# Kernel tuning notes

Hardware: AMD Instinct MI355X
Metric: run time of the kernel (lower is better)

The kernel has to match this reference:

```python
import jax, jax.numpy as jnp
import numpy as np

EMB = 768
NH = 12
DH = EMB // NH
NORM = float(np.sqrt(DH))  # 8.0


def setup_inputs() -> dict:
    key = jax.random.key(0)
    ks = jax.random.split(key, 9)
    B, S = 1, 4096
    s = 0.02  # realistic init scale for weights
    return {
        "x": jax.random.normal(ks[0], (B, S, EMB), jnp.float32),
        "mask": jnp.ones((B, S), jnp.float32),
        "Wq": jax.random.normal(ks[1], (EMB, EMB), jnp.float32) * s,
        "bq": jnp.zeros((EMB,), jnp.float32),
        "Wk": jax.random.normal(ks[2], (EMB, EMB), jnp.float32) * s,
        "bk": jnp.zeros((EMB,), jnp.float32),
        "Wv": jax.random.normal(ks[3], (EMB, EMB), jnp.float32) * s,
        "bv": jnp.zeros((EMB,), jnp.float32),
        "Wo": jax.random.normal(ks[4], (EMB, EMB), jnp.float32) * s,
        "bo": jnp.zeros((EMB,), jnp.float32),
    }


def reference(x, mask, Wq, bq, Wk, bk, Wv, bv, Wo, bo):
    B, S, _ = x.shape
    # QKV projections (torch Linear: x @ W.T + b)
    q = x @ Wq.T + bq
    k = x @ Wk.T + bk
    v = x @ Wv.T + bv
    # split heads: b s (nh dh) -> b nh s dh
    split = lambda t: t.reshape(B, S, NH, DH).transpose(0, 2, 1, 3)
    qh, kh, vh = split(q), split(k), split(v)
    # attention scores [b, nh, s, s]
    scores = jnp.einsum("bhqd,bhkd->bhqk", qh, kh) / NORM
    # additive mask: scores -= 10000 * (1 - mask), mask broadcast over query dim
    scores = scores - 10000.0 * (1.0 - mask[:, None, None, :])
    attn = jax.nn.softmax(scores, axis=-1)
    out = jnp.einsum("bhqk,bhkd->bhqd", attn, vh)
    # b nh s dh -> b s (nh dh)
    out = out.transpose(0, 2, 1, 3).reshape(B, S, EMB)
    return out @ Wo.T + bo
```

## Files before the change

### kernel.cpp

```cpp
#include <hip/hip_runtime.h>
#include <stdint.h>
#include <stddef.h>

#define EMB 768
#define SEQ 4096
#define NH 12
#define DH 64
#define LOG2E 1.44269504f
#define NSP 2
#define SPLEN (SEQ / NSP)
#define NBLK (NH * 32 * NSP)

typedef __attribute__((ext_vector_type(8))) short short8;
typedef __attribute__((ext_vector_type(4))) short short4v;
typedef __attribute__((ext_vector_type(4))) float f32x4;
typedef __attribute__((ext_vector_type(16))) float f32x16;
typedef __attribute__((ext_vector_type(2))) unsigned int uint32x2;

static __device__ __forceinline__ unsigned short f2bf(float f) {
  union { float f; uint32_t u; } v; v.f = f;
  uint32_t u = v.u;
  return (unsigned short)((u + 0x7FFFu + ((u >> 16) & 1u)) >> 16);
}
static __device__ __forceinline__ float bf2f(unsigned short s) {
  union { uint32_t u; float f; } v; v.u = ((uint32_t)s) << 16;
  return v.f;
}

static __device__ __forceinline__ void gl_lds16(const void* g, void* l) {
  __builtin_amdgcn_global_load_lds(
      (const __attribute__((address_space(1))) uint32_t*)g,
      (__attribute__((address_space(3))) uint32_t*)l, 16, 0, 0);
}
static __device__ __forceinline__ void gl_lds4(const void* g, void* l) {
  __builtin_amdgcn_global_load_lds(
      (const __attribute__((address_space(1))) uint32_t*)g,
      (__attribute__((address_space(3))) uint32_t*)l, 4, 0, 0);
}

__global__ void prep_kernel(const float* __restrict__ x, const float* __restrict__ mask,
                            const float* __restrict__ Wq, const float* __restrict__ Wk,
                            const float* __restrict__ Wv, const float* __restrict__ Wo,
                            unsigned short* __restrict__ xb, unsigned short* __restrict__ wqb,
                            unsigned short* __restrict__ wkb, unsigned short* __restrict__ wvb,
                            unsigned short* __restrict__ wob, float* __restrict__ mb2) {
  const int y = blockIdx.y;
  if (y == 5) {
    int i = blockIdx.x * 256 + threadIdx.x;
    if (i < SEQ) mb2[i] = -80000.f * (1.f - mask[i]);
    return;
  }
  const float* in = y == 0 ? x : y == 1 ? Wq : y == 2 ? Wk : y == 3 ? Wv : Wo;
  unsigned short* out = y == 0 ? xb : y == 1 ? wqb : y == 2 ? wkb : y == 3 ? wvb : wob;
  const int n = (y == 0) ? SEQ * EMB : EMB * EMB;
  int stride = gridDim.x * blockDim.x * 4;
  for (int i = (blockIdx.x * blockDim.x + threadIdx.x) * 4; i < n; i += stride) {
    float4 v = *reinterpret_cast<const float4*>(in + i);
    ushort4 o;
    o.x = f2bf(v.x); o.y = f2bf(v.y); o.z = f2bf(v.z); o.w = f2bf(v.w);
    *reinterpret_cast<ushort4*>(out + i) = o;
  }
}

template <int OUT_F32>
static __device__ __forceinline__ void gemm64(
    const unsigned short* __restrict__ A, const unsigned short* __restrict__ W,
    const float* __restrict__ bias, void* __restrict__ Cout,
    int M, int N, int K, int bm, int bn) {
  __shared__ unsigned short Alds[64 * 64];
  __shared__ unsigned short Blds[128 * 64];
  const int t = threadIdx.x;
  const int lane = t & 63;
  const int wave = t >> 6;
  const int wr = wave >> 1, wc = wave & 1;
  const int lm = lane & 15, lg = lane >> 4;

  f32x4 acc[2][4];
#pragma unroll
  for (int i = 0; i < 2; ++i)
#pragma unroll
    for (int j = 0; j < 4; ++j) acc[i][j] = (f32x4){0.f, 0.f, 0.f, 0.f};

  const int srow = t >> 3;
  const int scsw = (t & 7) * 16;

  const int nK = K >> 6;
  for (int kt = 0; kt < nK; ++kt) {
    const int k0 = kt << 6;
#pragma unroll
    for (int i = 0; i < 2; ++i) {
      int row = i * 32 + srow;
      int cb = scsw ^ ((row & 7) << 4);
      gl_lds16(A + (size_t)(bm * 64 + row) * K + k0 + (cb >> 1),
               (char*)Alds + i * 4096 + t * 16);
    }
#pragma unroll
    for (int i = 0; i < 4; ++i) {
      int row = i * 32 + srow;
      int cb = scsw ^ ((row & 7) << 4);
      gl_lds16(W + (size_t)(bn * 128 + row) * K + k0 + (cb >> 1),
               (char*)Blds + i * 4096 + t * 16);
    }
    __syncthreads();
#pragma unroll
    for (int kk = 0; kk < 2; ++kk) {
      short8 af[2], bfr[4];
#pragma unroll
      for (int i = 0; i < 2; ++i) {
        int rowa = wr * 32 + i * 16 + lm;
        int cba = (kk * 64 + lg * 16) ^ ((rowa & 7) << 4);
        af[i] = *reinterpret_cast<const short8*>((const char*)Alds + rowa * 128 + cba);
      }
#pragma unroll
      for (int j = 0; j < 4; ++j) {
        int rowb = wc * 64 + j * 16 + lm;
        int cbb = (kk * 64 + lg * 16) ^ ((rowb & 7) << 4);
        bfr[j] = *reinterpret_cast<const short8*>((const char*)Blds + rowb * 128 + cbb);
      }
#pragma unroll
      for (int i = 0; i < 2; ++i)
#pragma unroll
        for (int j = 0; j < 4; ++j)
          acc[i][j] = __builtin_amdgcn_mfma_f32_16x16x32_bf16(af[i], bfr[j], acc[i][j], 0, 0, 0);
    }
    __syncthreads();
  }
#pragma unroll
  for (int i = 0; i < 2; ++i) {
    int row0 = bm * 64 + wr * 32 + i * 16 + lg * 4;
#pragma unroll
    for (int j = 0; j < 4; ++j) {
      int col = bn * 128 + wc * 64 + j * 16 + lm;
      float b = bias[col];
#pragma unroll
      for (int r = 0; r < 4; ++r) {
        float v = acc[i][j][r] + b;
        if (OUT_F32)
          ((float*)Cout)[(size_t)(row0 + r) * N + col] = v;
        else
          ((unsigned short*)Cout)[(size_t)(row0 + r) * N + col] = f2bf(v);
      }
    }
  }
}

__global__ __launch_bounds__(256, 2) void gemm_wo(
    const unsigned short* __restrict__ A, const unsigned short* __restrict__ W,
    const float* __restrict__ bias, float* __restrict__ C) {
  gemm64<1>(A, W, bias, C, SEQ, EMB, EMB, blockIdx.x, blockIdx.y);
}

__global__ __launch_bounds__(256, 2) void qkv_gemm(
    const unsigned short* __restrict__ A,
    const unsigned short* __restrict__ W0, const unsigned short* __restrict__ W1,
    const unsigned short* __restrict__ W2,
    const float* __restrict__ b0, const float* __restrict__ b1, const float* __restrict__ b2,
    unsigned short* __restrict__ Qo, unsigned short* __restrict__ Ko,
    unsigned short* __restrict__ Vto) {
  __shared__ unsigned short smem[12288];
  unsigned short* Alds = smem;
  unsigned short* Blds = smem + 4096;

  const int z = blockIdx.z;
  const unsigned short* W = z == 0 ? W0 : z == 1 ? W1 : W2;
  const float* bias = z == 0 ? b0 : z == 1 ? b1 : b2;
  const int bm = blockIdx.x, bn = blockIdx.y;

  const int t = threadIdx.x;
  const int lane = t & 63;
  const int wave = t >> 6;
  const int wr = wave >> 1, wc = wave & 1;
  const int lm = lane & 15, lg = lane >> 4;

  f32x4 acc[2][4];
#pragma unroll
  for (int i = 0; i < 2; ++i)
#pragma unroll
    for (int j = 0; j < 4; ++j) acc[i][j] = (f32x4){0.f, 0.f, 0.f, 0.f};

  const int srow = t >> 3;
  const int scsw = (t & 7) * 16;

  for (int kt = 0; kt < EMB / 64; ++kt) {
    const int k0 = kt << 6;
#pragma unroll
    for (int i = 0; i < 2; ++i) {
      int row = i * 32 + srow;
      int cb = scsw ^ ((row & 7) << 4);
      gl_lds16(A + (size_t)(bm * 64 + row) * EMB + k0 + (cb >> 1),
               (char*)Alds + i * 4096 + t * 16);
    }
#pragma unroll
    for (int i = 0; i < 4; ++i) {
      int row = i * 32 + srow;
      int cb = scsw ^ ((row & 7) << 4);
      gl_lds16(W + (size_t)(bn * 128 + row) * EMB + k0 + (cb >> 1),
               (char*)Blds + i * 4096 + t * 16);
    }
    __syncthreads();
#pragma unroll
    for (int kk = 0; kk < 2; ++kk) {
      short8 af[2], bfr[4];
#pragma unroll
      for (int i = 0; i < 2; ++i) {
        int rowa = wr * 32 + i * 16 + lm;
        int cba = (kk * 64 + lg * 16) ^ ((rowa & 7) << 4);
        af[i] = *reinterpret_cast<const short8*>((const char*)Alds + rowa * 128 + cba);
      }
#pragma unroll
      for (int j = 0; j < 4; ++j) {
        int rowb = wc * 64 + j * 16 + lm;
        int cbb = (kk * 64 + lg * 16) ^ ((rowb & 7) << 4);
        bfr[j] = *reinterpret_cast<const short8*>((const char*)Blds + rowb * 128 + cbb);
      }
#pragma unroll
      for (int i = 0; i < 2; ++i)
#pragma unroll
        for (int j = 0; j < 4; ++j)
          acc[i][j] = __builtin_amdgcn_mfma_f32_16x16x32_bf16(af[i], bfr[j], acc[i][j], 0, 0, 0);
    }
    __syncthreads();
  }

  if (z < 2) {
    unsigned short* O = z == 0 ? Qo : Ko;
#pragma unroll
    for (int i = 0; i < 2; ++i) {
      int row0 = bm * 64 + wr * 32 + i * 16 + lg * 4;
#pragma unroll
      for (int j = 0; j < 4; ++j) {
        int col = bn * 128 + wc * 64 + j * 16 + lm;
        float b = bias[col];
#pragma unroll
        for (int r = 0; r < 4; ++r)
          O[(size_t)(row0 + r) * EMB + col] = f2bf(acc[i][j][r] + b);
      }
    }
  } else {
    unsigned short* T = smem;
#pragma unroll
    for (int i = 0; i < 2; ++i) {
      int rowL = wr * 32 + i * 16 + lg * 4;
#pragma unroll
      for (int j = 0; j < 4; ++j) {
        int colL = wc * 64 + j * 16 + lm;
        float b = bias[bn * 128 + colL];
        short4v s4;
#pragma unroll
        for (int r = 0; r < 4; ++r) s4[r] = (short)f2bf(acc[i][j][r] + b);
        *reinterpret_cast<short4v*>(T + colL * 72 + rowL) = s4;
      }
    }
    __syncthreads();
#pragma unroll
    for (int p = 0; p < 4; ++p) {
      int col = p * 32 + (t >> 3);
      int chunk = (t & 7) * 8;
      short8 v = *reinterpret_cast<const short8*>(T + col * 72 + chunk);
      *reinterpret_cast<short8*>(
          Vto + (size_t)(bn * 128 + col) * SEQ + bm * 64 + chunk) = v;
    }
  }
}

__global__ __launch_bounds__(256, 3) void attn_kernel(
    const unsigned short* __restrict__ Q, const unsigned short* __restrict__ Kb,
    const unsigned short* __restrict__ Vt, const float* __restrict__ mb2,
    unsigned short* __restrict__ opart, float* __restrict__ lpart) {
  __shared__ unsigned short Klds[2][64 * DH];
  __shared__ unsigned short Vlds[2][DH * 64];
  __shared__ __align__(16) float msk[2][64];

  const int t = threadIdx.x;
  const int lane = t & 63;
  const int wave = t >> 6;
  const int o = blockIdx.x;
  const int wg = (o & 7) * (NBLK / 8) + (o >> 3);
  const int head = wg >> 6;
  const int rem = wg & 63;
  const int qb = rem >> 1;
  const int sp = rem & 1;
  const int q0 = qb * 128 + wave * 32;
  const int kvb0 = sp * SPLEN;
  const int lm = lane & 31;
  const int h = lane >> 5;

  const float sc2 = 0.125f * LOG2E;
  const float mfix = 32.0f;

  short8 qf[4];
#pragma unroll
  for (int ks = 0; ks < 4; ++ks)
    qf[ks] = *reinterpret_cast<const short8*>(
        Q + (size_t)(q0 + lm) * EMB + head * DH + ks * 16 + h * 8);

  short8 ones;
#pragma unroll
  for (int i = 0; i < 8; ++i) ones[i] = (short)0x3F80;

  f32x16 oacc[2], lacc;
#pragma unroll
  for (int n = 0; n < 2; ++n)
#pragma unroll
    for (int r = 0; r < 16; ++r) oacc[n][r] = 0.f;
#pragma unroll
  for (int r = 0; r < 16; ++r) lacc[r] = 0.f;

  const int srow = t >> 3;
  const int scol = (t & 7) * 16;

  auto STAGE = [&](int buf, int kt2) {
    const int kv0 = kvb0 + kt2 * 64;
#pragma unroll
    for (int i = 0; i < 2; ++i) {
      int row = i * 32 + srow;
      int cb = scol ^ ((row & 7) << 4);
      gl_lds16(Kb + (size_t)(kv0 + row) * EMB + head * DH + (cb >> 1),
               (char*)Klds + buf * 8192 + i * 4096 + t * 16);
      gl_lds16(Vt + (size_t)(head * DH + row) * SEQ + kv0 + (cb >> 1),
               (char*)Vlds + buf * 8192 + i * 4096 + t * 16);
    }
    gl_lds4(mb2 + kv0 + lane, &msk[buf][0]);
  };

  constexpr int NT = SPLEN / 64;
  STAGE(0, 0);
  __syncthreads();

  for (int kt = 0; kt < NT; ++kt) {
    const int buf = kt & 1;
    if (kt + 1 < NT) STAGE(buf ^ 1, kt + 1);

    f32x16 s[2];
#pragma unroll
    for (int tt = 0; tt < 2; ++tt)
#pragma unroll
      for (int a = 0; a < 4; ++a) {
        f32x4 m = *reinterpret_cast<const f32x4*>(&msk[buf][tt * 32 + a * 8 + h * 4]);
#pragma unroll
        for (int i = 0; i < 4; ++i) s[tt][a * 4 + i] = m[i];
      }

    __builtin_amdgcn_s_setprio(1);
#pragma unroll
    for (int tt = 0; tt < 2; ++tt)
#pragma unroll
      for (int ks = 0; ks < 4; ++ks) {
        int row = tt * 32 + lm;
        int cb = (ks * 32 + h * 16) ^ ((row & 7) << 4);
        short8 kf = *reinterpret_cast<const short8*>(
            (const char*)Klds + buf * 8192 + row * 128 + cb);
        s[tt] = __builtin_amdgcn_mfma_f32_32x32x16_bf16(kf, qf[ks], s[tt], 0, 0, 0);
      }
    __builtin_amdgcn_s_setprio(0);

#pragma unroll
    for (int tt = 0; tt < 2; ++tt)
#pragma unroll
      for (int r = 0; r < 16; ++r)
        s[tt][r] = __builtin_amdgcn_exp2f(fmaf(s[tt][r], sc2, -mfix));

    short8 pa[4];
#pragma unroll
    for (int tt = 0; tt < 2; ++tt) {
      uint32_t r0[4], r1[4];
#pragma unroll
      for (int a = 0; a < 4; ++a) {
        asm("v_cvt_pk_bf16_f32 %0, %1, %2" : "=v"(r0[a]) : "v"(s[tt][4 * a]), "v"(s[tt][4 * a + 1]));
        asm("v_cvt_pk_bf16_f32 %0, %1, %2" : "=v"(r1[a]) : "v"(s[tt][4 * a + 2]), "v"(s[tt][4 * a + 3]));
      }
#pragma unroll
      for (int ksl = 0; ksl < 2; ++ksl) {
        uint32x2 w0 = __builtin_amdgcn_permlane32_swap(r0[2 * ksl], r0[2 * ksl + 1], false, false);
        uint32x2 w1 = __builtin_amdgcn_permlane32_swap(r1[2 * ksl], r1[2 * ksl + 1], false, false);
        union { short8 s8; uint32_t u[4]; } pk;
        pk.u[0] = w0[0]; pk.u[1] = w1[0]; pk.u[2] = w0[1]; pk.u[3] = w1[1];
        pa[tt * 2 + ksl] = pk.s8;
      }
    }

    __builtin_amdgcn_s_setprio(1);
#pragma unroll
    for (int n = 0; n < 2; ++n)
#pragma unroll
      for (int ks = 0; ks < 4; ++ks) {
        int row = n * 32 + lm;
        int cb = (ks * 32 + h * 16) ^ ((row & 7) << 4);
        short8 vf = *reinterpret_cast<const short8*>(
            (const char*)Vlds + buf * 8192 + row * 128 + cb);
        oacc[n] = __builtin_amdgcn_mfma_f32_32x32x16_bf16(pa[ks], vf, oacc[n], 0, 0, 0);
      }
#pragma unroll
    for (int ks = 0; ks < 4; ++ks)
      lacc = __builtin_amdgcn_mfma_f32_32x32x16_bf16(pa[ks], ones, lacc, 0, 0, 0);
    __builtin_amdgcn_s_setprio(0);

    __syncthreads();
  }

  f32x16 rl;
#pragma unroll
  for (int r = 0; r < 16; ++r) rl[r] = __builtin_amdgcn_rcpf(lacc[r]);
  unsigned short* ob = opart + ((size_t)(sp * NH + head) * SEQ + q0) * 64;
#pragma unroll
  for (int n = 0; n < 2; ++n)
#pragma unroll
    for (int r = 0; r < 16; ++r) {
      int crow = (r & 3) + 8 * (r >> 2) + 4 * h;
      ob[crow * 64 + n * 32 + lm] = f2bf(oacc[n][r] * rl[r]);
    }
  const size_t pbase = (size_t)(sp * NH + head) * SEQ + q0;
  if (lm == 0) {
#pragma unroll
    for (int r = 0; r < 16; ++r) {
      int crow = (r & 3) + 8 * (r >> 2) + 4 * h;
      lpart[pbase + crow] = lacc[r];
    }
  }
}

__global__ void merge_kernel(const unsigned short* __restrict__ opart,
                             const float* __restrict__ lpart,
                             unsigned short* __restrict__ Ab) {
  int tid = blockIdx.x * 256 + threadIdx.x;
  int dv = tid & 15;
  int rq = tid >> 4;
  int head = rq >> 12;
  int q = rq & 4095;
  size_t base = (size_t)head * SEQ + q;
  const size_t str = (size_t)NH * SEQ;

  float l0 = lpart[base], l1 = lpart[base + str];
  float rd = 1.0f / (l0 + l1);
  float c0 = l0 * rd, c1 = l1 * rd;

  ushort4 o0 = *reinterpret_cast<const ushort4*>(opart + base * 64 + dv * 4);
  ushort4 o1 = *reinterpret_cast<const ushort4*>(opart + (base + str) * 64 + dv * 4);
  ushort4 r;
  r.x = f2bf(c0 * bf2f(o0.x) + c1 * bf2f(o1.x));
  r.y = f2bf(c0 * bf2f(o0.y) + c1 * bf2f(o1.y));
  r.z = f2bf(c0 * bf2f(o0.z) + c1 * bf2f(o1.z));
  r.w = f2bf(c0 * bf2f(o0.w) + c1 * bf2f(o1.w));
  *reinterpret_cast<ushort4*>(Ab + (size_t)q * EMB + head * DH + dv * 4) = r;
}

extern "C" void kernel_launch(void* const* d_in, const int* in_sizes, int n_in,
                              void* d_out, int out_size, void* d_ws, size_t ws_size,
                              hipStream_t stream) {
  const float* x    = (const float*)d_in[0];
  const float* mask = (const float*)d_in[1];
  const float* Wq   = (const float*)d_in[2];
  const float* bq   = (const float*)d_in[3];
  const float* Wk   = (const float*)d_in[4];
  const float* bk   = (const float*)d_in[5];
  const float* Wv   = (const float*)d_in[6];
  const float* bv   = (const float*)d_in[7];
  const float* Wo   = (const float*)d_in[8];
  const float* bo   = (const float*)d_in[9];
  float* out = (float*)d_out;

  char* ws = (char*)d_ws;
  const size_t SZ_X = (size_t)SEQ * EMB * 2;
  const size_t SZ_W = (size_t)EMB * EMB * 2;
  unsigned short* xb  = (unsigned short*)(ws);
  unsigned short* wqb = (unsigned short*)(ws + SZ_X);
  unsigned short* wkb = (unsigned short*)(ws + SZ_X + SZ_W);
  unsigned short* wvb = (unsigned short*)(ws + SZ_X + 2 * SZ_W);
  unsigned short* wob = (unsigned short*)(ws + SZ_X + 3 * SZ_W);
  unsigned short* Qb  = (unsigned short*)(ws + SZ_X + 4 * SZ_W);
  unsigned short* Kbuf= (unsigned short*)(ws + 2 * SZ_X + 4 * SZ_W);
  unsigned short* Vtb = (unsigned short*)(ws + 3 * SZ_X + 4 * SZ_W);
  unsigned short* Ab  = (unsigned short*)(ws + 4 * SZ_X + 4 * SZ_W);
  size_t off = 5 * SZ_X + 4 * SZ_W;
  float* mb2            = (float*)(ws + off);          off += (size_t)SEQ * 4;
  unsigned short* opart = (unsigned short*)(ws + off); off += (size_t)NSP * NH * SEQ * 64 * 2;
  float* lpart          = (float*)(ws + off);

  prep_kernel<<<dim3(192, 6), 256, 0, stream>>>(
      x, mask, Wq, Wk, Wv, Wo, xb, wqb, wkb, wvb, wob, mb2);

  qkv_gemm<<<dim3(SEQ / 64, EMB / 128, 3), 256, 0, stream>>>(
      xb, wqb, wkb, wvb, bq, bk, bv, Qb, Kbuf, Vtb);

  attn_kernel<<<NBLK, 256, 0, stream>>>(Qb, Kbuf, Vtb, mb2, opart, lpart);

  merge_kernel<<<3072, 256, 0, stream>>>(opart, lpart, Ab);

  gemm_wo<<<dim3(SEQ / 64, EMB / 128), 256, 0, stream>>>(Ab, wob, bo, out);
}
```

Measured before the change: 119.0 us.

## Use 512-thread attention blocks with 256-query tiles and 4-way KV split

Attention blocks grow to 8 waves covering 256 queries, so each K/V tile staged in LDS is shared by twice as many query rows. The KV sequence is split into 4 parts instead of 2 to keep the block count unchanged, and the merge kernel is generalised to combine NSP partial outputs. Staging now issues one load per thread per tile because there are twice as many threads. The costs are double the partial-output traffic in the merge, a tighter per-thread register budget under the new launch bounds, and a shorter KV loop per block.

```diff
diff --git a/kernel.cpp b/kernel.cpp
--- a/kernel.cpp
+++ b/kernel.cpp
@@ -7,9 +7,10 @@
 #define NH 12
 #define DH 64
 #define LOG2E 1.44269504f
-#define NSP 2
+#define NSP 4
 #define SPLEN (SEQ / NSP)
-#define NBLK (NH * 32 * NSP)
+#define QBLK 256
+#define NBLK (NH * (SEQ / QBLK) * NSP)
 
 typedef __attribute__((ext_vector_type(8))) short short8;
 typedef __attribute__((ext_vector_type(4))) short short4v;
@@ -263,7 +264,7 @@
   }
 }
 
-__global__ __launch_bounds__(256, 3) void attn_kernel(
+__global__ __launch_bounds__(512, 6) void attn_kernel(
     const unsigned short* __restrict__ Q, const unsigned short* __restrict__ Kb,
     const unsigned short* __restrict__ Vt, const float* __restrict__ mb2,
     unsigned short* __restrict__ opart, float* __restrict__ lpart) {
@@ -278,9 +279,9 @@
   const int wg = (o & 7) * (NBLK / 8) + (o >> 3);
   const int head = wg >> 6;
   const int rem = wg & 63;
-  const int qb = rem >> 1;
-  const int sp = rem & 1;
-  const int q0 = qb * 128 + wave * 32;
+  const int qb = rem >> 2;
+  const int sp = rem & 3;
+  const int q0 = qb * QBLK + wave * 32;
   const int kvb0 = sp * SPLEN;
   const int lm = lane & 31;
   const int h = lane >> 5;
@@ -311,15 +312,11 @@
 
   auto STAGE = [&](int buf, int kt2) {
     const int kv0 = kvb0 + kt2 * 64;
-#pragma unroll
-    for (int i = 0; i < 2; ++i) {
-      int row = i * 32 + srow;
-      int cb = scol ^ ((row & 7) << 4);
-      gl_lds16(Kb + (size_t)(kv0 + row) * EMB + head * DH + (cb >> 1),
-               (char*)Klds + buf * 8192 + i * 4096 + t * 16);
-      gl_lds16(Vt + (size_t)(head * DH + row) * SEQ + kv0 + (cb >> 1),
-               (char*)Vlds + buf * 8192 + i * 4096 + t * 16);
-    }
+    int cb = scol ^ ((srow & 7) << 4);
+    gl_lds16(Kb + (size_t)(kv0 + srow) * EMB + head * DH + (cb >> 1),
+             (char*)Klds + buf * 8192 + t * 16);
+    gl_lds16(Vt + (size_t)(head * DH + srow) * SEQ + kv0 + (cb >> 1),
+             (char*)Vlds + buf * 8192 + t * 16);
     gl_lds4(mb2 + kv0 + lane, &msk[buf][0]);
   };
 
@@ -430,17 +427,27 @@
   size_t base = (size_t)head * SEQ + q;
   const size_t str = (size_t)NH * SEQ;
 
-  float l0 = lpart[base], l1 = lpart[base + str];
-  float rd = 1.0f / (l0 + l1);
-  float c0 = l0 * rd, c1 = l1 * rd;
-
-  ushort4 o0 = *reinterpret_cast<const ushort4*>(opart + base * 64 + dv * 4);
-  ushort4 o1 = *reinterpret_cast<const ushort4*>(opart + (base + str) * 64 + dv * 4);
+  float l[NSP], denom = 0.f;
+#pragma unroll
+  for (int sp = 0; sp < NSP; ++sp) {
+    l[sp] = lpart[base + sp * str];
+    denom += l[sp];
+  }
+  float rd = 1.0f / denom;
+
+  float a0 = 0.f, a1 = 0.f, a2 = 0.f, a3 = 0.f;
+#pragma unroll
+  for (int sp = 0; sp < NSP; ++sp) {
+    float c = l[sp] * rd;
+    ushort4 ov = *reinterpret_cast<const ushort4*>(
+        opart + (base + sp * str) * 64 + dv * 4);
+    a0 += c * bf2f(ov.x);
+    a1 += c * bf2f(ov.y);
+    a2 += c * bf2f(ov.z);
+    a3 += c * bf2f(ov.w);
+  }
   ushort4 r;
-  r.x = f2bf(c0 * bf2f(o0.x) + c1 * bf2f(o1.x));
-  r.y = f2bf(c0 * bf2f(o0.y) + c1 * bf2f(o1.y));
-  r.z = f2bf(c0 * bf2f(o0.z) + c1 * bf2f(o1.z));
-  r.w = f2bf(c0 * bf2f(o0.w) + c1 * bf2f(o1.w));
+  r.x = f2bf(a0); r.y = f2bf(a1); r.z = f2bf(a2); r.w = f2bf(a3);
   *reinterpret_cast<ushort4*>(Ab + (size_t)q * EMB + head * DH + dv * 4) = r;
 }
 
@@ -482,7 +489,7 @@
   qkv_gemm<<<dim3(SEQ / 64, EMB / 128, 3), 256, 0, stream>>>(
       xb, wqb, wkb, wvb, bq, bk, bv, Qb, Kbuf, Vtb);
 
-  attn_kernel<<<NBLK, 256, 0, stream>>>(Qb, Kbuf, Vtb, mb2, opart, lpart);
+  attn_kernel<<<NBLK, 512, 0, stream>>>(Qb, Kbuf, Vtb, mb2, opart, lpart);
 
   merge_kernel<<<3072, 256, 0, stream>>>(opart, lpart, Ab);
 
```

New measurement: 445.1 us. 3.74x slower.
